# Performance work log

Measured on AMD Instinct MI355X. Metric: run time of the kernel, lower is better.

The kernel has to match this reference:

```python
import jax, jax.numpy as jnp
import numpy as np

NUM_CLASSES = 80
ANCHORS = np.array([[10,13],[16,30],[33,23],[30,61],[62,45],[59,119],[116,90],[156,198],[373,326]], np.float32)
MASK = [[0,1,2],[3,4,5],[6,7,8]]
STRIDES = [8, 16, 32]
MAX_OUT = 100      # max_output_size_per_class == max_total_size
IOU_THR = 0.45
SCORE_THR = 0.25
NMS_TOPK = 128     # per-class candidate pre-selection for greedy NMS (>= MAX_OUT)


def setup_inputs() -> dict:
    key = jax.random.key(0)
    k1, k2, k3 = jax.random.split(key, 3)
    B = 16
    C = 3 * (NUM_CLASSES + 5)  # 255
    return {
        'p3': jax.random.normal(k1, (B, 80, 80, C), jnp.float32),
        'p4': jax.random.normal(k2, (B, 40, 40, C), jnp.float32),
        'p5': jax.random.normal(k3, (B, 20, 20, C), jnp.float32),
    }


def _decode(logits, anchors, stride):
    # logits: [B,H,W,3*(nc+5)] -> boxes [B,H*W*3,4] (x1y1x2y2), obj [B,M], cls [B,M,nc]
    B, H, W, _ = logits.shape
    A = anchors.shape[0]
    x = logits.reshape(B, H, W, A, NUM_CLASSES + 5)
    xy = jax.nn.sigmoid(x[..., :2])
    wh_logit = x[..., 2:4]
    obj = jax.nn.sigmoid(x[..., 4])
    cls = jax.nn.sigmoid(x[..., 5:])
    gx, gy = jnp.meshgrid(jnp.arange(W, dtype=x.dtype), jnp.arange(H, dtype=x.dtype))
    grid = jnp.stack([gx, gy], axis=-1)[:, :, None, :]  # [H,W,1,2]
    ctr = (xy + grid) * stride
    wh = jnp.exp(wh_logit) * anchors  # [B,H,W,A,2]
    box = jnp.concatenate([ctr - wh / 2.0, ctr + wh / 2.0], axis=-1)
    return box.reshape(B, -1, 4), obj.reshape(B, -1), cls.reshape(B, -1, NUM_CLASSES)


def _pairwise_iou(b):
    # b: [K,4] x1y1x2y2 -> [K,K]
    area = (b[:, 2] - b[:, 0]) * (b[:, 3] - b[:, 1])
    lt = jnp.maximum(b[:, None, :2], b[None, :, :2])
    rb = jnp.minimum(b[:, None, 2:], b[None, :, 2:])
    wh = jnp.clip(rb - lt, 0.0)
    inter = wh[..., 0] * wh[..., 1]
    return inter / (area[:, None] + area[None, :] - inter + 1e-9)


def _nms_single(boxes, scores):
    # boxes [N,4], scores [N] for one (image, class): greedy NMS on top-K candidates
    s = jnp.where(scores > SCORE_THR, scores, -1.0)
    top_s, idx = jax.lax.top_k(s, NMS_TOPK)   # sorted descending
    b = boxes[idx]                            # [K,4]
    iou = _pairwise_iou(b)                    # [K,K]
    rng = jnp.arange(NMS_TOPK)

    def body(keep, i):
        active = keep[i] & (top_s[i] > 0.0)
        sup = active & (iou[i] > IOU_THR) & (rng > i)
        return keep & ~sup, None

    keep, _ = jax.lax.scan(body, jnp.ones(NMS_TOPK, bool), rng)
    valid = keep & (top_s > 0.0)
    ss = jnp.where(valid, top_s, -1.0)
    sel_s, sel_i = jax.lax.top_k(ss, MAX_OUT)
    return b[sel_i], sel_s                    # [M,4], [M]


def _per_image(boxes, scores_cn):
    # boxes [N,4] shared across classes (q=1), scores_cn [C,N]
    cb, cs = jax.vmap(_nms_single, in_axes=(None, 0))(boxes, scores_cn)  # [C,M,4],[C,M]
    C = cs.shape[0]
    cls_id = jnp.broadcast_to(jnp.arange(C, dtype=boxes.dtype)[:, None], cs.shape)
    fs, fi = jax.lax.top_k(cs.reshape(-1), MAX_OUT)
    fb = cb.reshape(-1, 4)[fi]
    fc = cls_id.reshape(-1)[fi]
    valid = fs > 0.0
    n_valid = jnp.sum(valid).astype(jnp.int32)
    return (jnp.where(valid[:, None], fb, 0.0),
            jnp.where(valid, fs, 0.0),
            jnp.where(valid, fc, 0.0),
            n_valid)


def _forward(p3, p4, p5):
    boxes, objs, clss = [], [], []
    for logits, m, stride in zip((p3, p4, p5), MASK, STRIDES):
        b, o, c = _decode(logits, jnp.asarray(ANCHORS[m]), float(stride))
        boxes.append(b); objs.append(o); clss.append(c)
    boxes = jnp.concatenate(boxes, axis=1)   # [B,N,4]
    obj = jnp.concatenate(objs, axis=1)      # [B,N]
    cls = jnp.concatenate(clss, axis=1)      # [B,N,C]
    scores = obj[..., None] * cls            # [B,N,C]
    return jax.vmap(_per_image)(boxes, scores.transpose(0, 2, 1))


def reference(p3, p4, p5):
    # returns (boxes [B,100,4], scores [B,100], classes [B,100], valid [B])
    return _forward(p3, p4, p5)
```

## Files before the change

### kernel.cpp

```cpp
#include <hip/hip_runtime.h>
#include <stdint.h>

#define NUM_CLASSES 80
#define N_ANCH 25200
#define B_IMG 16
#define NMS_TOPK_ 128
#define MAX_OUT_ 100
#define SCORE_THR_ 0.25f
#define IOU_THR_ 0.45f
#define NBINS 2048
#define CAP 2048
#define CAPB 1024
#define CAPC 256
#define U8_BASE 0x3E7Eu
#define TILES_PER_IMG 394

__constant__ float c_anch[9][2] = {
    {10.f, 13.f}, {16.f, 30.f}, {33.f, 23.f},
    {30.f, 61.f}, {62.f, 45.f}, {59.f, 119.f},
    {116.f, 90.f}, {156.f, 198.f}, {373.f, 326.f}};

__device__ __forceinline__ float sigmoidf_(float x) {
    return 1.0f / (1.0f + expf(-x));
}

__device__ __forceinline__ float fast_sigmoid_(float x) {
    float t = __expf(-x);
    return __fdividef(1.0f, 1.0f + t);
}

__device__ __forceinline__ unsigned int score_u8_(float s) {
    unsigned int u = __float_as_uint(s) >> 16;
    int bin = (int)u - (int)U8_BASE;
    if (bin < 0) bin = 0;
    if (bin > 255) bin = 255;
    return (unsigned int)bin;
}

__device__ __forceinline__ unsigned int score_bin(unsigned int bits) {
    unsigned int bin = (bits - 0x3E800000u) >> 13;
    if (bin >= NBINS) bin = NBINS - 1;
    return bin;
}


__global__ void __launch_bounds__(256) decode_tile_kernel(
    const float* __restrict__ p3, const float* __restrict__ p4,
    const float* __restrict__ p5, float* __restrict__ boxes,
    unsigned char* __restrict__ score_u8) {
    int blk = blockIdx.x;
    int b = blk / TILES_PER_IMG;
    int tile = blk - b * TILES_PER_IMG;
    const float* p; int W, lvl, il0, base, ta;
    if (tile < 300)      { p = p3; W = 80; lvl = 0; il0 = tile * 64;         base = 0;     ta = 64; }
    else if (tile < 375) { p = p4; W = 40; lvl = 1; il0 = (tile - 300) * 64; base = 19200; ta = 64; }
    else                 { p = p5; W = 20; lvl = 2; il0 = (tile - 375) * 64; base = 24000;
                           ta = (tile == 393) ? 48 : 64; }
    float stride = (float)(8 << lvl);

    __shared__ float raw[64 * 85];
    int tid = threadIdx.x;

    {
        const float4* src4 = (const float4*)(p + (size_t)b * ((size_t)W * W * 255) +
                                             (size_t)il0 * 85);
        float4* raw4 = (float4*)raw;
        int n4 = ta * 85 / 4;
        for (int k = tid; k < n4; k += 256) raw4[k] = src4[k];
    }
    __syncthreads();

    int wave = tid >> 6;
    int lane = tid & 63;

    if (lane < 16) {
        int a = wave * 16 + lane;
        if (a < ta) {
            int il = il0 + a;
            int y = il / (W * 3);
            int t = il - y * (W * 3);
            int x = t / 3;
            int an = t - x * 3;
            const float* q = &raw[a * 85];
            float cx = (sigmoidf_(q[0]) + (float)x) * stride;
            float cy = (sigmoidf_(q[1]) + (float)y) * stride;
            float bw = expf(q[2]) * c_anch[lvl * 3 + an][0];
            float bh = expf(q[3]) * c_anch[lvl * 3 + an][1];
            float4 bo = {cx - bw * 0.5f, cy - bh * 0.5f,
                         cx + bw * 0.5f, cy + bh * 0.5f};
            *(float4*)(boxes + ((size_t)b * N_ANCH + base + il) * 4) = bo;
        }
    }

    if (lane < ta) {
        const float* q = &raw[lane * 85];
        float obj = fast_sigmoid_(q[4]);
        size_t sb = (size_t)b * NUM_CLASSES * N_ANCH + (size_t)(base + il0 + lane);
#pragma unroll
        for (int it = 0; it < 20; ++it) {
            int c = wave * 20 + it;
            float s = obj * fast_sigmoid_(q[5 + c]);
            score_u8[sb + (size_t)c * N_ANCH] = (unsigned char)score_u8_(s);
        }
    }
}

__global__ void __launch_bounds__(256) select_topk_u8_kernel(
    const unsigned char* __restrict__ score_u8,
    const float* __restrict__ p3, const float* __restrict__ p4,
    const float* __restrict__ p5,
    unsigned long long* __restrict__ topsel) {
    int bc = blockIdx.x;
    int b = bc / NUM_CLASSES;
    int c = bc - b * NUM_CLASSES;
    int tid = threadIdx.x;
    int wave = tid >> 6;
    const uint4* sc = (const uint4*)(score_u8 + (size_t)bc * N_ANCH);

    __shared__ unsigned int hist[4][256];
    __shared__ unsigned long long sel[CAPB];
    __shared__ unsigned int s_cnt;
    __shared__ int s_cut;

#pragma unroll
    for (int wv = 0; wv < 4; ++wv) hist[wv][tid & 255] = 0u;
    if (tid == 0) s_cnt = 0u;
    __syncthreads();

    unsigned int* myhist = hist[wave];
    for (int i = tid; i < N_ANCH / 16; i += 256) {
        uint4 v = sc[i];
        unsigned int ww[4] = {v.x, v.y, v.z, v.w};
#pragma unroll
        for (int k = 0; k < 16; ++k) {
            unsigned int bin = (ww[k >> 2] >> ((k & 3) * 8)) & 0xFFu;
            if (bin) atomicAdd(&myhist[bin], 1u);
        }
    }
    __syncthreads();

    {
        unsigned int m = hist[0][tid] + hist[1][tid] + hist[2][tid] + hist[3][tid];
        hist[0][tid] = m;
    }
    __syncthreads();

    if (tid == 0) {
        unsigned int tot = 0; int cut = 0;
        for (int t = 255; t >= 1; --t) {
            tot += hist[0][t];
            if (tot >= NMS_TOPK_) { cut = t; break; }
        }
        s_cut = cut;
    }
    __syncthreads();
    int coll = s_cut - 1;
    if (coll < 1) coll = 1;

    for (int i = tid; i < N_ANCH / 16; i += 256) {
        uint4 v = sc[i];
        unsigned int ww[4] = {v.x, v.y, v.z, v.w};
#pragma unroll
        for (int k = 0; k < 16; ++k) {
            unsigned int bin = (ww[k >> 2] >> ((k & 3) * 8)) & 0xFFu;
            if ((int)bin >= coll) {
                unsigned int pos = atomicAdd(&s_cnt, 1u);
                if (pos < CAPB) sel[pos] = (unsigned long long)(i * 16 + k);
            }
        }
    }
    __syncthreads();

    unsigned int M = s_cnt;
    if (M > CAPB) M = CAPB;

    for (unsigned int t = tid; t < M; t += 256) {
        unsigned int idx = (unsigned int)sel[t];
        const float* q;
        if (idx < 19200u)      q = p3 + (size_t)b * 1632000 + (size_t)idx * 85;
        else if (idx < 24000u) q = p4 + (size_t)b * 408000 + (size_t)(idx - 19200u) * 85;
        else                   q = p5 + (size_t)b * 102000 + (size_t)(idx - 24000u) * 85;
        float s = sigmoidf_(q[4]) * sigmoidf_(q[5 + c]);
        sel[t] = (s > SCORE_THR_)
                     ? (((unsigned long long)__float_as_uint(s) << 32) |
                        (unsigned long long)(~idx))
                     : 0ull;
    }
    __syncthreads();

    unsigned int P2 = 1;
    while (P2 < M) P2 <<= 1;
    if (P2 < 2) P2 = 2;
    for (unsigned int k = M + tid; k < P2; k += 256) sel[k] = 0ull;
    __syncthreads();

    for (unsigned int k = 2; k <= P2; k <<= 1) {
        for (unsigned int j = k >> 1; j > 0; j >>= 1) {
            for (unsigned int t = tid; t < (int)P2; t += 256) {
                unsigned int ixj = (unsigned int)t ^ j;
                if (ixj > (unsigned int)t) {
                    unsigned long long a0 = sel[t], b0 = sel[ixj];
                    bool desc = (((unsigned int)t & k) == 0);
                    if (desc ? (a0 < b0) : (a0 > b0)) { sel[t] = b0; sel[ixj] = a0; }
                }
            }
            __syncthreads();
        }
    }

    unsigned long long* dst = topsel + (size_t)bc * NMS_TOPK_;
    if (tid < NMS_TOPK_) dst[tid] = ((unsigned int)tid < M) ? sel[tid] : 0ull;
}

__global__ void __launch_bounds__(64) nms_kernel(
    const unsigned long long* __restrict__ topsel,
    const float* __restrict__ boxes,
    float* __restrict__ cls_score, float* __restrict__ cls_box) {
    int bc = blockIdx.x;
    int b = bc / NUM_CLASSES;
    unsigned int lane = threadIdx.x;

    __shared__ float bx[NMS_TOPK_][8];

    const unsigned long long* src = topsel + (size_t)bc * NMS_TOPK_;
    unsigned long long e0 = src[lane];
    unsigned long long e1 = src[64 + lane];

    bool k0 = (e0 != 0ull);
    bool k1 = (e1 != 0ull);

    float x00 = 0, y00 = 0, x01 = 0, y01 = 0, a0 = 0, sv0 = 0;
    float x10 = 0, y10 = 0, x11 = 0, y11 = 0, a1 = 0, sv1 = 0;
    if (k0) {
        unsigned int idx = ~((unsigned int)(e0 & 0xFFFFFFFFull));
        float4 bp = *(const float4*)(boxes + ((size_t)b * N_ANCH + idx) * 4);
        x00 = bp.x; y00 = bp.y; x01 = bp.z; y01 = bp.w;
        sv0 = __uint_as_float((unsigned int)(e0 >> 32));
        a0 = (x01 - x00) * (y01 - y00);
    }
    if (k1) {
        unsigned int idx = ~((unsigned int)(e1 & 0xFFFFFFFFull));
        float4 bp = *(const float4*)(boxes + ((size_t)b * N_ANCH + idx) * 4);
        x10 = bp.x; y10 = bp.y; x11 = bp.z; y11 = bp.w;
        sv1 = __uint_as_float((unsigned int)(e1 >> 32));
        a1 = (x11 - x10) * (y11 - y10);
    }
    {
        float4 v0 = {x00, y00, x01, y01};
        float4 v1 = {x10, y10, x11, y11};
        *(float4*)&bx[lane][0] = v0;
        *(float4*)&bx[64 + lane][0] = v1;
    }
    __syncthreads();

    unsigned long long km0 = __ballot(k0);
    unsigned long long km1 = __ballot(k1);
    for (unsigned int i = 0; i < NMS_TOPK_; ++i) {
        bool ki = ((((i < 64) ? km0 : km1) >> (i & 63)) & 1ull) != 0ull;
        if (ki) {
            float4 rb = *(const float4*)&bx[i][0];
            float ra = (rb.z - rb.x) * (rb.w - rb.y);
            if (k0 && lane > i) {
                float lx = fmaxf(rb.x, x00), ly = fmaxf(rb.y, y00);
                float rx = fminf(rb.z, x01), ry = fminf(rb.w, y01);
                float w = fmaxf(rx - lx, 0.f), h = fmaxf(ry - ly, 0.f);
                float inter = w * h;
                float iou = inter / (ra + a0 - inter + 1e-9f);
                if (iou > IOU_THR_) k0 = false;
            }
            if (k1 && (64 + lane) > i) {
                float lx = fmaxf(rb.x, x10), ly = fmaxf(rb.y, y10);
                float rx = fminf(rb.z, x11), ry = fminf(rb.w, y11);
                float w = fmaxf(rx - lx, 0.f), h = fmaxf(ry - ly, 0.f);
                float inter = w * h;
                float iou = inter / (ra + a1 - inter + 1e-9f);
                if (iou > IOU_THR_) k1 = false;
            }
            km0 = __ballot(k0);
            km1 = __ballot(k1);
        }
    }

    float* scd = cls_score + (size_t)bc * MAX_OUT_;
    float* bod = cls_box + (size_t)bc * (MAX_OUT_ * 4);
    int n0 = __popcll(km0);
    int n = n0 + __popcll(km1);
    if (k0) {
        int pos = __popcll(km0 & ((1ull << lane) - 1ull));
        if (pos < MAX_OUT_) {
            scd[pos] = sv0;
            bod[pos * 4 + 0] = x00; bod[pos * 4 + 1] = y00;
            bod[pos * 4 + 2] = x01; bod[pos * 4 + 3] = y01;
        }
    }
    if (k1) {
        int pos = n0 + __popcll(km1 & ((1ull << lane) - 1ull));
        if (pos < MAX_OUT_) {
            scd[pos] = sv1;
            bod[pos * 4 + 0] = x10; bod[pos * 4 + 1] = y10;
            bod[pos * 4 + 2] = x11; bod[pos * 4 + 3] = y11;
        }
    }
    int start = n < MAX_OUT_ ? n : MAX_OUT_;
    for (int p2 = start + (int)lane; p2 < MAX_OUT_; p2 += 64) {
        scd[p2] = -1.0f;
        bod[p2 * 4 + 0] = 0.f; bod[p2 * 4 + 1] = 0.f;
        bod[p2 * 4 + 2] = 0.f; bod[p2 * 4 + 3] = 0.f;
    }
}

__global__ void __launch_bounds__(256) final_fast_kernel(
    const float* __restrict__ cls_score, const float* __restrict__ cls_box,
    float* __restrict__ out) {
    int b = blockIdx.x;
    int tid = threadIdx.x;
    const int NC = NUM_CLASSES * MAX_OUT_;
    const float* sc = cls_score + (size_t)b * NC;

    __shared__ unsigned int hist[NBINS];
    __shared__ unsigned int segsum[256];
    __shared__ unsigned long long keys[CAPC];
    __shared__ unsigned int s_cnt, s_tot;
    __shared__ int s_cut;

    for (int k = tid; k < NBINS; k += 256) hist[k] = 0u;
    if (tid == 0) s_cnt = 0u;
    __syncthreads();

    for (int k = tid; k < NC; k += 256) {
        float s = sc[k];
        if (s > 0.0f) atomicAdd(&hist[score_bin(__float_as_uint(s))], 1u);
    }
    __syncthreads();

    unsigned int ss = 0;
    for (int k = 0; k < 8; ++k) ss += hist[tid * 8 + k];
    segsum[tid] = ss;
    __syncthreads();
    if (tid == 0) {
        unsigned int total = 0;
        for (int t = 0; t < 256; ++t) total += segsum[t];
        s_tot = total;
        unsigned int tot = 0; int cut = 0; int t = 255;
        for (; t >= 0; --t) {
            if (tot + segsum[t] >= MAX_OUT_) break;
            tot += segsum[t];
        }
        if (t >= 0) {
            int j = 7;
            for (; j >= 0; --j) { tot += hist[t * 8 + j]; if (tot >= MAX_OUT_) break; }
            if (j < 0) j = 0;
            cut = t * 8 + j;
        }
        s_cut = cut;
    }
    __syncthreads();
    unsigned int cutoff = (unsigned int)s_cut;

    for (int k = tid; k < NC; k += 256) {
        float s = sc[k];
        if (s > 0.0f && score_bin(__float_as_uint(s)) >= cutoff) {
            unsigned int pos = atomicAdd(&s_cnt, 1u);
            if (pos < CAPC) {
                keys[pos] = ((unsigned long long)__float_as_uint(s) << 32) |
                            (unsigned long long)(~(unsigned int)k);
            }
        }
    }
    __syncthreads();

    unsigned int M = s_cnt;
    if (M > CAPC) M = CAPC;
    unsigned int P2 = 1;
    while (P2 < M) P2 <<= 1;
    if (P2 < 2) P2 = 2;
    for (unsigned int k = M + tid; k < P2; k += 256) keys[k] = 0ull;
    __syncthreads();

    for (unsigned int k = 2; k <= P2; k <<= 1) {
        for (unsigned int j = k >> 1; j > 0; j >>= 1) {
            for (unsigned int t = (unsigned int)tid; t < P2; t += 256) {
                unsigned int ixj = t ^ j;
                if (ixj > t) {
                    unsigned long long a0 = keys[t], b0 = keys[ixj];
                    bool desc = ((t & k) == 0);
                    if (desc ? (a0 < b0) : (a0 > b0)) { keys[t] = b0; keys[ixj] = a0; }
                }
            }
            __syncthreads();
        }
    }

    float* ob = out;
    float* os = out + B_IMG * MAX_OUT_ * 4;
    float* oc = os + B_IMG * MAX_OUT_;
    float* on = oc + B_IMG * MAX_OUT_;

    unsigned int K = M < MAX_OUT_ ? M : MAX_OUT_;
    if (tid < MAX_OUT_) {
        if ((unsigned int)tid < K) {
            unsigned long long kk = keys[tid];
            unsigned int flat = ~((unsigned int)(kk & 0xFFFFFFFFull));
            float sv = __uint_as_float((unsigned int)(kk >> 32));
            const float* bp = cls_box + ((size_t)b * NC + flat) * 4;
            os[b * MAX_OUT_ + tid] = sv;
            oc[b * MAX_OUT_ + tid] = (float)(flat / MAX_OUT_);
            ob[(b * MAX_OUT_ + tid) * 4 + 0] = bp[0];
            ob[(b * MAX_OUT_ + tid) * 4 + 1] = bp[1];
            ob[(b * MAX_OUT_ + tid) * 4 + 2] = bp[2];
            ob[(b * MAX_OUT_ + tid) * 4 + 3] = bp[3];
        } else {
            os[b * MAX_OUT_ + tid] = 0.0f;
            oc[b * MAX_OUT_ + tid] = 0.0f;
            ob[(b * MAX_OUT_ + tid) * 4 + 0] = 0.0f;
            ob[(b * MAX_OUT_ + tid) * 4 + 1] = 0.0f;
            ob[(b * MAX_OUT_ + tid) * 4 + 2] = 0.0f;
            ob[(b * MAX_OUT_ + tid) * 4 + 3] = 0.0f;
        }
    }
    if (tid == 0) {
        unsigned int nv = s_tot < MAX_OUT_ ? s_tot : MAX_OUT_;
        on[b] = (float)nv;
    }
}


__global__ void __launch_bounds__(256) decode_kernel(
    const float* __restrict__ p3, const float* __restrict__ p4,
    const float* __restrict__ p5, float* __restrict__ boxes,
    float* __restrict__ obj) {
    int gid = blockIdx.x * blockDim.x + threadIdx.x;
    if (gid >= B_IMG * N_ANCH) return;
    int b = gid / N_ANCH;
    int i = gid - b * N_ANCH;
    const float* p; int W, il, lvl; float stride;
    if (i < 19200)      { p = p3; W = 80; il = i;         lvl = 0; stride = 8.f;  }
    else if (i < 24000) { p = p4; W = 40; il = i - 19200; lvl = 1; stride = 16.f; }
    else                { p = p5; W = 20; il = i - 24000; lvl = 2; stride = 32.f; }
    int y = il / (W * 3);
    int t = il - y * W * 3;
    int x = t / 3;
    int a = t - x * 3;
    const float* q = p + ((((size_t)b * W + y) * W + x) * 255 + a * 85);
    float cx = (sigmoidf_(q[0]) + (float)x) * stride;
    float cy = (sigmoidf_(q[1]) + (float)y) * stride;
    float bw = expf(q[2]) * c_anch[lvl * 3 + a][0];
    float bh = expf(q[3]) * c_anch[lvl * 3 + a][1];
    float* bo = boxes + (size_t)gid * 4;
    bo[0] = cx - bw * 0.5f; bo[1] = cy - bh * 0.5f;
    bo[2] = cx + bw * 0.5f; bo[3] = cy + bh * 0.5f;
    obj[gid] = sigmoidf_(q[4]);
}

__device__ __forceinline__ float cand_score(
    const float* __restrict__ p3, const float* __restrict__ p4,
    const float* __restrict__ p5, const float* __restrict__ obj,
    int b, int c, int i) {
    const float* p; int W, il;
    if (i < 19200)      { p = p3; W = 80; il = i;         }
    else if (i < 24000) { p = p4; W = 40; il = i - 19200; }
    else                { p = p5; W = 20; il = i - 24000; }
    int y = il / (W * 3);
    int t = il - y * W * 3;
    int x = t / 3;
    int a = t - x * 3;
    float cl = p[(((size_t)b * W + y) * W + x) * 255 + a * 85 + 5 + c];
    return obj[b * N_ANCH + i] * sigmoidf_(cl);
}

__global__ void __launch_bounds__(256) topk_nms_kernel(
    const float* __restrict__ p3, const float* __restrict__ p4,
    const float* __restrict__ p5, const float* __restrict__ boxes,
    const float* __restrict__ obj, float* __restrict__ cls_score,
    float* __restrict__ cls_box) {
    int b = blockIdx.x / NUM_CLASSES;
    int c = blockIdx.x % NUM_CLASSES;
    int tid = threadIdx.x;

    __shared__ unsigned int hist[NBINS];
    __shared__ unsigned long long keys[CAP];
    __shared__ unsigned int s_cnt, s_cutoff;
    __shared__ float bx[NMS_TOPK_][5];
    __shared__ float bs[NMS_TOPK_];
    __shared__ int keep[NMS_TOPK_];

    for (int k = tid; k < NBINS; k += 256) hist[k] = 0u;
    if (tid == 0) s_cnt = 0u;
    __syncthreads();

    for (int i = tid; i < N_ANCH; i += 256) {
        float s = cand_score(p3, p4, p5, obj, b, c, i);
        if (s > SCORE_THR_) atomicAdd(&hist[score_bin(__float_as_uint(s))], 1u);
    }
    __syncthreads();

    if (tid == 0) {
        unsigned int total = 0;
        int cut = 0;
        for (int k = NBINS - 1; k >= 0; --k) {
            total += hist[k];
            if (total >= NMS_TOPK_) { cut = k; break; }
        }
        s_cutoff = (unsigned int)cut;
    }
    __syncthreads();
    unsigned int cutoff = s_cutoff;

    for (int i = tid; i < N_ANCH; i += 256) {
        float s = cand_score(p3, p4, p5, obj, b, c, i);
        if (s > SCORE_THR_) {
            unsigned int bits = __float_as_uint(s);
            if (score_bin(bits) >= cutoff) {
                unsigned int pos = atomicAdd(&s_cnt, 1u);
                if (pos < CAP) {
                    keys[pos] = ((unsigned long long)bits << 32) |
                                (unsigned long long)(~(unsigned int)i);
                }
            }
        }
    }
    __syncthreads();

    unsigned int M = s_cnt;
    if (M > CAP) M = CAP;
    unsigned int P2 = 1;
    while (P2 < M) P2 <<= 1;
    if (P2 < 2) P2 = 2;
    for (unsigned int k = M + tid; k < P2; k += 256) keys[k] = 0ull;
    __syncthreads();

    for (unsigned int k = 2; k <= P2; k <<= 1) {
        for (unsigned int j = k >> 1; j > 0; j >>= 1) {
            for (unsigned int t = tid; t < P2; t += 256) {
                unsigned int ixj = t ^ j;
                if (ixj > t) {
                    unsigned long long a0 = keys[t], b0 = keys[ixj];
                    bool desc = ((t & k) == 0);
                    if (desc ? (a0 < b0) : (a0 > b0)) { keys[t] = b0; keys[ixj] = a0; }
                }
            }
            __syncthreads();
        }
    }

    unsigned int K = M < NMS_TOPK_ ? M : NMS_TOPK_;
    if (tid < (int)K) {
        unsigned long long kk = keys[tid];
        unsigned int idx = ~((unsigned int)(kk & 0xFFFFFFFFull));
        const float* bp = boxes + ((size_t)b * N_ANCH + idx) * 4;
        bx[tid][0] = bp[0]; bx[tid][1] = bp[1];
        bx[tid][2] = bp[2]; bx[tid][3] = bp[3];
        bs[tid] = __uint_as_float((unsigned int)(kk >> 32));
        keep[tid] = 1;
    }
    __syncthreads();

    for (unsigned int i = 0; i < K; ++i) {
        if (keep[i]) {
            unsigned int t = (unsigned int)tid;
            if (t > i && t < K && keep[t]) {
                float ax0 = bx[i][0], ay0 = bx[i][1], ax1 = bx[i][2], ay1 = bx[i][3];
                float cx0 = bx[t][0], cy0 = bx[t][1], cx1 = bx[t][2], cy1 = bx[t][3];
                float areaA = (ax1 - ax0) * (ay1 - ay0);
                float areaB = (cx1 - cx0) * (cy1 - cy0);
                float lx = fmaxf(ax0, cx0), ly = fmaxf(ay0, cy0);
                float rx = fminf(ax1, cx1), ry = fminf(ay1, cy1);
                float w = rx - lx; if (w < 0.f) w = 0.f;
                float h = ry - ly; if (h < 0.f) h = 0.f;
                float inter = w * h;
                float iou = inter / (areaA + areaB - inter + 1e-9f);
                if (iou > IOU_THR_) keep[t] = 0;
            }
        }
        __syncthreads();
    }

    if (tid == 0) {
        float* scd = cls_score + ((size_t)b * NUM_CLASSES + c) * MAX_OUT_;
        float* bod = cls_box + ((size_t)b * NUM_CLASSES + c) * MAX_OUT_ * 4;
        int out_n = 0;
        for (unsigned int t2 = 0; t2 < K && out_n < MAX_OUT_; ++t2) {
            if (keep[t2]) {
                scd[out_n] = bs[t2];
                bod[out_n * 4 + 0] = bx[t2][0];
                bod[out_n * 4 + 1] = bx[t2][1];
                bod[out_n * 4 + 2] = bx[t2][2];
                bod[out_n * 4 + 3] = bx[t2][3];
                out_n++;
            }
        }
        for (; out_n < MAX_OUT_; ++out_n) {
            scd[out_n] = -1.0f;
            bod[out_n * 4 + 0] = 0.f; bod[out_n * 4 + 1] = 0.f;
            bod[out_n * 4 + 2] = 0.f; bod[out_n * 4 + 3] = 0.f;
        }
    }
}

extern "C" void kernel_launch(void* const* d_in, const int* in_sizes, int n_in,
                              void* d_out, int out_size, void* d_ws, size_t ws_size,
                              hipStream_t stream) {
    const float* p3 = (const float*)d_in[0];
    const float* p4 = (const float*)d_in[1];
    const float* p5 = (const float*)d_in[2];

    const size_t boxesB  = (size_t)B_IMG * N_ANCH * 4 * sizeof(float);
    const size_t clsSB   = (size_t)B_IMG * NUM_CLASSES * MAX_OUT_ * sizeof(float);
    const size_t clsBB   = clsSB * 4;
    const size_t topselB = (size_t)B_IMG * NUM_CLASSES * NMS_TOPK_ * 8;
    const size_t scoreUB = (size_t)B_IMG * NUM_CLASSES * N_ANCH;
    const size_t need_new = boxesB + clsSB + clsBB + topselB + scoreUB;

    char* base = (char*)d_ws;

    if (ws_size >= need_new) {
        float* boxes     = (float*)base;
        float* cls_score = (float*)(base + boxesB);
        float* cls_box   = (float*)(base + boxesB + clsSB);
        unsigned long long* topsel =
            (unsigned long long*)(base + boxesB + clsSB + clsBB);
        unsigned char* score_u8 =
            (unsigned char*)(base + boxesB + clsSB + clsBB + topselB);

        decode_tile_kernel<<<B_IMG * TILES_PER_IMG, 256, 0, stream>>>(
            p3, p4, p5, boxes, score_u8);
        select_topk_u8_kernel<<<B_IMG * NUM_CLASSES, 256, 0, stream>>>(
            score_u8, p3, p4, p5, topsel);
        nms_kernel<<<B_IMG * NUM_CLASSES, 64, 0, stream>>>(
            topsel, boxes, cls_score, cls_box);
        final_fast_kernel<<<B_IMG, 256, 0, stream>>>(cls_score, cls_box, (float*)d_out);
    } else {
        float* boxes = (float*)base;
        float* obj = boxes + (size_t)B_IMG * N_ANCH * 4;
        float* cls_score = obj + (size_t)B_IMG * N_ANCH;
        float* cls_box = cls_score + (size_t)B_IMG * NUM_CLASSES * MAX_OUT_;

        int tot = B_IMG * N_ANCH;
        decode_kernel<<<(tot + 255) / 256, 256, 0, stream>>>(p3, p4, p5, boxes, obj);
        topk_nms_kernel<<<B_IMG * NUM_CLASSES, 256, 0, stream>>>(
            p3, p4, p5, boxes, obj, cls_score, cls_box);
        final_fast_kernel<<<B_IMG, 256, 0, stream>>>(cls_score, cls_box, (float*)d_out);
    }
}
```

Measured before the change: 295.2 us.

## Decode boxes lazily in NMS, use coarse-range histogram in top-k select

The decode kernel no longer writes a full box array; NMS decodes its candidate boxes directly from the raw logits. This removes a large global write and later read, at the cost of redundant scattered decodes of the same anchor across classes. The top-k select kernel first counts scores into 8 coarse ranges using per-thread registers and wave reductions, then builds the fine atomic histogram only for the range holding the cutoff, which cuts LDS atomic contention. The final kernel uses per-wave histograms to spread atomics.

```diff
diff --git a/kernel.cpp b/kernel.cpp
--- a/kernel.cpp
+++ b/kernel.cpp
@@ -43,20 +43,43 @@
     return bin;
 }
 
-
-__global__ void __launch_bounds__(256) decode_tile_kernel(
+__device__ __forceinline__ float4 decode_box_(
     const float* __restrict__ p3, const float* __restrict__ p4,
-    const float* __restrict__ p5, float* __restrict__ boxes,
-    unsigned char* __restrict__ score_u8) {
+    const float* __restrict__ p5, int b, unsigned int idx) {
+    const float* p; int W, lvl, il;
+    if (idx < 19200u)      { p = p3; W = 80; lvl = 0; il = (int)idx; }
+    else if (idx < 24000u) { p = p4; W = 40; lvl = 1; il = (int)idx - 19200; }
+    else                   { p = p5; W = 20; lvl = 2; il = (int)idx - 24000; }
+    float stride = (float)(8 << lvl);
+    int y = il / (W * 3);
+    int t = il - y * (W * 3);
+    int x = t / 3;
+    int a = t - x * 3;
+    const float* q = p + (size_t)b * ((size_t)W * W * 255) + (size_t)il * 85;
+    float cx = (sigmoidf_(q[0]) + (float)x) * stride;
+    float cy = (sigmoidf_(q[1]) + (float)y) * stride;
+    float bw = expf(q[2]) * c_anch[lvl * 3 + a][0];
+    float bh = expf(q[3]) * c_anch[lvl * 3 + a][1];
+    return make_float4(cx - bw * 0.5f, cy - bh * 0.5f,
+                       cx + bw * 0.5f, cy + bh * 0.5f);
+}
+
+#define WRED_(r) { r += __shfl_xor(r, 1); r += __shfl_xor(r, 2); \
+                   r += __shfl_xor(r, 4); r += __shfl_xor(r, 8); \
+                   r += __shfl_xor(r, 16); r += __shfl_xor(r, 32); }
+
+
+__global__ void __launch_bounds__(256) decode_score_kernel(
+    const float* __restrict__ p3, const float* __restrict__ p4,
+    const float* __restrict__ p5, unsigned char* __restrict__ score_u8) {
     int blk = blockIdx.x;
     int b = blk / TILES_PER_IMG;
     int tile = blk - b * TILES_PER_IMG;
-    const float* p; int W, lvl, il0, base, ta;
-    if (tile < 300)      { p = p3; W = 80; lvl = 0; il0 = tile * 64;         base = 0;     ta = 64; }
-    else if (tile < 375) { p = p4; W = 40; lvl = 1; il0 = (tile - 300) * 64; base = 19200; ta = 64; }
-    else                 { p = p5; W = 20; lvl = 2; il0 = (tile - 375) * 64; base = 24000;
+    const float* p; int W, il0, base, ta;
+    if (tile < 300)      { p = p3; W = 80; il0 = tile * 64;         base = 0;     ta = 64; }
+    else if (tile < 375) { p = p4; W = 40; il0 = (tile - 300) * 64; base = 19200; ta = 64; }
+    else                 { p = p5; W = 20; il0 = (tile - 375) * 64; base = 24000;
                            ta = (tile == 393) ? 48 : 64; }
-    float stride = (float)(8 << lvl);
 
     __shared__ float raw[64 * 85];
     int tid = threadIdx.x;
@@ -72,25 +95,6 @@
 
     int wave = tid >> 6;
     int lane = tid & 63;
-
-    if (lane < 16) {
-        int a = wave * 16 + lane;
-        if (a < ta) {
-            int il = il0 + a;
-            int y = il / (W * 3);
-            int t = il - y * (W * 3);
-            int x = t / 3;
-            int an = t - x * 3;
-            const float* q = &raw[a * 85];
-            float cx = (sigmoidf_(q[0]) + (float)x) * stride;
-            float cy = (sigmoidf_(q[1]) + (float)y) * stride;
-            float bw = expf(q[2]) * c_anch[lvl * 3 + an][0];
-            float bh = expf(q[3]) * c_anch[lvl * 3 + an][1];
-            float4 bo = {cx - bw * 0.5f, cy - bh * 0.5f,
-                         cx + bw * 0.5f, cy + bh * 0.5f};
-            *(float4*)(boxes + ((size_t)b * N_ANCH + base + il) * 4) = bo;
-        }
-    }
 
     if (lane < ta) {
         const float* q = &raw[lane * 85];
@@ -115,55 +119,104 @@
     int c = bc - b * NUM_CLASSES;
     int tid = threadIdx.x;
     int wave = tid >> 6;
+    int lane = tid & 63;
     const uint4* sc = (const uint4*)(score_u8 + (size_t)bc * N_ANCH);
 
+    __shared__ unsigned int rng[8];
     __shared__ unsigned int hist[4][256];
     __shared__ unsigned long long sel[CAPB];
-    __shared__ unsigned int s_cnt;
-    __shared__ int s_cut;
-
+    __shared__ unsigned int s_cnt, s_base;
+    __shared__ int s_cut, s_lo, s_hi;
+
+    if (tid < 8) rng[tid] = 0u;
 #pragma unroll
     for (int wv = 0; wv < 4; ++wv) hist[wv][tid & 255] = 0u;
     if (tid == 0) s_cnt = 0u;
     __syncthreads();
 
-    unsigned int* myhist = hist[wave];
+    {
+        unsigned int r0 = 0, r1 = 0, r2 = 0, r3 = 0, r4 = 0, r5 = 0, r6 = 0, r7 = 0;
+        for (int i = tid; i < N_ANCH / 16; i += 256) {
+            uint4 v = sc[i];
+            unsigned int ww[4] = {v.x, v.y, v.z, v.w};
+#pragma unroll
+            for (int k = 0; k < 16; ++k) {
+                unsigned int b8 = (ww[k >> 2] >> ((k & 3) * 8)) & 0xFFu;
+                if (b8 >= 128u) {
+                    if (b8 >= 192u) { if (b8 >= 224u) ++r7; else ++r6; }
+                    else            { if (b8 >= 160u) ++r5; else ++r4; }
+                } else if (b8) {
+                    if (b8 >= 64u)  { if (b8 >= 96u)  ++r3; else ++r2; }
+                    else            { if (b8 >= 32u)  ++r1; else ++r0; }
+                }
+            }
+        }
+        WRED_(r0) WRED_(r1) WRED_(r2) WRED_(r3)
+        WRED_(r4) WRED_(r5) WRED_(r6) WRED_(r7)
+        if (lane == 0) {
+            atomicAdd(&rng[0], r0); atomicAdd(&rng[1], r1);
+            atomicAdd(&rng[2], r2); atomicAdd(&rng[3], r3);
+            atomicAdd(&rng[4], r4); atomicAdd(&rng[5], r5);
+            atomicAdd(&rng[6], r6); atomicAdd(&rng[7], r7);
+        }
+    }
+    __syncthreads();
+
+    if (tid == 0) {
+        unsigned int cum = 0; int j = -1;
+        for (int k = 7; k >= 0; --k) {
+            cum += rng[k];
+            if (cum >= NMS_TOPK_) { j = k; break; }
+        }
+        if (j < 0) {
+            s_cut = 1; s_lo = 256; s_hi = 256; s_base = 0u;
+        } else {
+            s_lo = (j == 0) ? 1 : (32 * j);
+            s_hi = 32 * (j + 1);
+            s_base = cum - rng[j];
+            s_cut = (j == 0) ? 1 : (32 * j);
+        }
+    }
+    __syncthreads();
+
+    if (s_lo < 256) {
+        int lo = s_lo, hi = s_hi;
+        unsigned int* myhist = hist[wave];
+        for (int i = tid; i < N_ANCH / 16; i += 256) {
+            uint4 v = sc[i];
+            unsigned int ww[4] = {v.x, v.y, v.z, v.w};
+#pragma unroll
+            for (int k = 0; k < 16; ++k) {
+                int bin = (int)((ww[k >> 2] >> ((k & 3) * 8)) & 0xFFu);
+                if (bin >= lo && bin < hi) atomicAdd(&myhist[bin], 1u);
+            }
+        }
+        __syncthreads();
+        {
+            unsigned int m = hist[0][tid] + hist[1][tid] + hist[2][tid] + hist[3][tid];
+            hist[0][tid] = m;
+        }
+        __syncthreads();
+        if (tid == 0) {
+            unsigned int tot = s_base; int cut = s_lo;
+            for (int t = s_hi - 1; t >= s_lo; --t) {
+                tot += hist[0][t];
+                if (tot >= NMS_TOPK_) { cut = t; break; }
+            }
+            s_cut = cut;
+        }
+        __syncthreads();
+    }
+    int coll = s_cut - 1;
+    if (coll < 1) coll = 1;
+
     for (int i = tid; i < N_ANCH / 16; i += 256) {
         uint4 v = sc[i];
         unsigned int ww[4] = {v.x, v.y, v.z, v.w};
 #pragma unroll
         for (int k = 0; k < 16; ++k) {
-            unsigned int bin = (ww[k >> 2] >> ((k & 3) * 8)) & 0xFFu;
-            if (bin) atomicAdd(&myhist[bin], 1u);
-        }
-    }
-    __syncthreads();
-
-    {
-        unsigned int m = hist[0][tid] + hist[1][tid] + hist[2][tid] + hist[3][tid];
-        hist[0][tid] = m;
-    }
-    __syncthreads();
-
-    if (tid == 0) {
-        unsigned int tot = 0; int cut = 0;
-        for (int t = 255; t >= 1; --t) {
-            tot += hist[0][t];
-            if (tot >= NMS_TOPK_) { cut = t; break; }
-        }
-        s_cut = cut;
-    }
-    __syncthreads();
-    int coll = s_cut - 1;
-    if (coll < 1) coll = 1;
-
-    for (int i = tid; i < N_ANCH / 16; i += 256) {
-        uint4 v = sc[i];
-        unsigned int ww[4] = {v.x, v.y, v.z, v.w};
-#pragma unroll
-        for (int k = 0; k < 16; ++k) {
-            unsigned int bin = (ww[k >> 2] >> ((k & 3) * 8)) & 0xFFu;
-            if ((int)bin >= coll) {
+            int bin = (int)((ww[k >> 2] >> ((k & 3) * 8)) & 0xFFu);
+            if (bin >= coll) {
                 unsigned int pos = atomicAdd(&s_cnt, 1u);
                 if (pos < CAPB) sel[pos] = (unsigned long long)(i * 16 + k);
             }
@@ -214,7 +267,8 @@
 
 __global__ void __launch_bounds__(64) nms_kernel(
     const unsigned long long* __restrict__ topsel,
-    const float* __restrict__ boxes,
+    const float* __restrict__ p3, const float* __restrict__ p4,
+    const float* __restrict__ p5,
     float* __restrict__ cls_score, float* __restrict__ cls_box) {
     int bc = blockIdx.x;
     int b = bc / NUM_CLASSES;
@@ -233,14 +287,14 @@
     float x10 = 0, y10 = 0, x11 = 0, y11 = 0, a1 = 0, sv1 = 0;
     if (k0) {
         unsigned int idx = ~((unsigned int)(e0 & 0xFFFFFFFFull));
-        float4 bp = *(const float4*)(boxes + ((size_t)b * N_ANCH + idx) * 4);
+        float4 bp = decode_box_(p3, p4, p5, b, idx);
         x00 = bp.x; y00 = bp.y; x01 = bp.z; y01 = bp.w;
         sv0 = __uint_as_float((unsigned int)(e0 >> 32));
         a0 = (x01 - x00) * (y01 - y00);
     }
     if (k1) {
         unsigned int idx = ~((unsigned int)(e1 & 0xFFFFFFFFull));
-        float4 bp = *(const float4*)(boxes + ((size_t)b * N_ANCH + idx) * 4);
+        float4 bp = decode_box_(p3, p4, p5, b, idx);
         x10 = bp.x; y10 = bp.y; x11 = bp.z; y11 = bp.w;
         sv1 = __uint_as_float((unsigned int)(e1 >> 32));
         a1 = (x11 - x10) * (y11 - y10);
@@ -314,27 +368,35 @@
     float* __restrict__ out) {
     int b = blockIdx.x;
     int tid = threadIdx.x;
+    int wave = tid >> 6;
     const int NC = NUM_CLASSES * MAX_OUT_;
     const float* sc = cls_score + (size_t)b * NC;
 
-    __shared__ unsigned int hist[NBINS];
+    __shared__ unsigned int hist[4][NBINS];
     __shared__ unsigned int segsum[256];
     __shared__ unsigned long long keys[CAPC];
     __shared__ unsigned int s_cnt, s_tot;
     __shared__ int s_cut;
 
-    for (int k = tid; k < NBINS; k += 256) hist[k] = 0u;
+    for (int k = tid; k < NBINS; k += 256) {
+        hist[0][k] = 0u; hist[1][k] = 0u; hist[2][k] = 0u; hist[3][k] = 0u;
+    }
     if (tid == 0) s_cnt = 0u;
     __syncthreads();
 
+    unsigned int* myhist = hist[wave];
     for (int k = tid; k < NC; k += 256) {
         float s = sc[k];
-        if (s > 0.0f) atomicAdd(&hist[score_bin(__float_as_uint(s))], 1u);
+        if (s > 0.0f) atomicAdd(&myhist[score_bin(__float_as_uint(s))], 1u);
+    }
+    __syncthreads();
+    for (int k = tid; k < NBINS; k += 256) {
+        hist[0][k] = hist[0][k] + hist[1][k] + hist[2][k] + hist[3][k];
     }
     __syncthreads();
 
     unsigned int ss = 0;
-    for (int k = 0; k < 8; ++k) ss += hist[tid * 8 + k];
+    for (int k = 0; k < 8; ++k) ss += hist[0][tid * 8 + k];
     segsum[tid] = ss;
     __syncthreads();
     if (tid == 0) {
@@ -348,7 +410,7 @@
         }
         if (t >= 0) {
             int j = 7;
-            for (; j >= 0; --j) { tot += hist[t * 8 + j]; if (tot >= MAX_OUT_) break; }
+            for (; j >= 0; --j) { tot += hist[0][t * 8 + j]; if (tot >= MAX_OUT_) break; }
             if (j < 0) j = 0;
             cut = t * 8 + j;
         }
@@ -604,30 +666,28 @@
     const float* p4 = (const float*)d_in[1];
     const float* p5 = (const float*)d_in[2];
 
-    const size_t boxesB  = (size_t)B_IMG * N_ANCH * 4 * sizeof(float);
     const size_t clsSB   = (size_t)B_IMG * NUM_CLASSES * MAX_OUT_ * sizeof(float);
     const size_t clsBB   = clsSB * 4;
     const size_t topselB = (size_t)B_IMG * NUM_CLASSES * NMS_TOPK_ * 8;
     const size_t scoreUB = (size_t)B_IMG * NUM_CLASSES * N_ANCH;
-    const size_t need_new = boxesB + clsSB + clsBB + topselB + scoreUB;
+    const size_t need_new = clsSB + clsBB + topselB + scoreUB;
 
     char* base = (char*)d_ws;
 
     if (ws_size >= need_new) {
-        float* boxes     = (float*)base;
-        float* cls_score = (float*)(base + boxesB);
-        float* cls_box   = (float*)(base + boxesB + clsSB);
+        float* cls_score = (float*)base;
+        float* cls_box   = (float*)(base + clsSB);
         unsigned long long* topsel =
-            (unsigned long long*)(base + boxesB + clsSB + clsBB);
+            (unsigned long long*)(base + clsSB + clsBB);
         unsigned char* score_u8 =
-            (unsigned char*)(base + boxesB + clsSB + clsBB + topselB);
-
-        decode_tile_kernel<<<B_IMG * TILES_PER_IMG, 256, 0, stream>>>(
-            p3, p4, p5, boxes, score_u8);
+            (unsigned char*)(base + clsSB + clsBB + topselB);
+
+        decode_score_kernel<<<B_IMG * TILES_PER_IMG, 256, 0, stream>>>(
+            p3, p4, p5, score_u8);
         select_topk_u8_kernel<<<B_IMG * NUM_CLASSES, 256, 0, stream>>>(
             score_u8, p3, p4, p5, topsel);
         nms_kernel<<<B_IMG * NUM_CLASSES, 64, 0, stream>>>(
-            topsel, boxes, cls_score, cls_box);
+            topsel, p3, p4, p5, cls_score, cls_box);
         final_fast_kernel<<<B_IMG, 256, 0, stream>>>(cls_score, cls_box, (float*)d_out);
     } else {
         float* boxes = (float*)base;
```

Result: slower. 320.9 us (+8.7%).
